# Kernel optimization log

Hardware: AMD Instinct MI355X
Metric: run time of the kernel (lower is better)

The kernel has to match this reference:

```python
import jax, jax.numpy as jnp
import numpy as np
from jax import lax

S = 8  # num_segments


def conv2d(x, w, stride=1, pad=0):
    return lax.conv_general_dilated(x, w, (stride, stride), [(pad, pad), (pad, pad)],
                                    dimension_numbers=('NCHW', 'OIHW', 'NCHW'))


def bn(x, g, b):  # inference-mode BatchNorm as per-channel affine
    return x * g[None, :, None, None] + b[None, :, None, None]


def conv1x1(x, w):  # w: [O, C]
    return jnp.einsum('bchw,oc->bohw', x, w)


def avgpool3s2(x):  # AvgPool2d(3, stride=2, padding=1), count_include_pad=True
    s = lax.reduce_window(x, 0.0, lax.add, (1, 1, 3, 3), (1, 1, 2, 2),
                          [(0, 0), (0, 0), (1, 1), (1, 1)])
    return s / 9.0


def navigation_mask(x, gumbel, nav_w, nav_bn_g, nav_bn_b, gs_w, gs_b, temp=1.0):
    B = x.shape[0]
    y = x.mean(axis=(2, 3))                                    # global avg pool -> [B, C]
    g = jnp.maximum(y @ nav_w.T * nav_bn_g + nav_bn_b, 0.0)    # conv_pool (1x1) + BN + ReLU -> [B, 2]
    g = g.reshape(B // S, S, 2)
    # grouped 1x1 conv (groups=S) == per-segment 2x2 matmul; gs_w: [S, out, in]
    logits = jnp.einsum('bsi,sji->bsj', g, gs_w) + gs_b        # [nvid, S, 2]
    y_soft = jax.nn.softmax((logits + gumbel) / temp, axis=-1)
    hard = jax.nn.one_hot(jnp.argmax(y_soft, axis=-1), 2, dtype=y_soft.dtype)
    y_st = hard + y_soft - lax.stop_gradient(y_soft)           # straight-through hard gumbel
    return y_st[:, :, 1].reshape(B, 1, 1, 1)                   # channel 1 = focal-on


def setup_inputs() -> dict:
    key = jax.random.key(0)
    ks = iter(jax.random.split(key, 48))

    def rn(shape, scale=0.05):
        return jax.random.normal(next(ks), shape, dtype=jnp.float32) * scale

    B, C_in, C_out, C_amp, H = 128, 64, 128, 64, 56
    u = jax.random.uniform(next(ks), (B // S, S, 2), minval=1e-6, maxval=1.0 - 1e-6)
    return dict(
        x=rn((B, C_in, H, H), 1.0),
        gumbel=(-jnp.log(-jnp.log(u))).astype(jnp.float32),
        nav_w=rn((2, C_in)), nav_bn_g=jnp.ones((2,), jnp.float32), nav_bn_b=jnp.zeros((2,), jnp.float32),
        gs_w=rn((S, 2, 2)),
        gs_b=jnp.tile(jnp.array([1.0, 10.0], dtype=jnp.float32), (S, 1)),  # bias init from source
        ba_w1=rn((C_amp, C_in, 3, 3)), ba_g1=jnp.ones((C_amp,), jnp.float32), ba_b1=jnp.zeros((C_amp,), jnp.float32),
        ba_w2=rn((C_amp, C_amp, 3, 3)), ba_g2=jnp.ones((C_amp,), jnp.float32), ba_b2=jnp.zeros((C_amp,), jnp.float32),
        bf_wd=rn((C_out, C_in)), bf_gd=jnp.ones((C_out,), jnp.float32), bf_bd=jnp.zeros((C_out,), jnp.float32),
        bf_w1=rn((C_out, C_in, 3, 3)), bf_g1=jnp.ones((C_out,), jnp.float32), bf_b1=jnp.zeros((C_out,), jnp.float32),
        bf_w2=rn((C_out, C_out, 3, 3)), bf_g2=jnp.ones((C_out,), jnp.float32), bf_b2=jnp.zeros((C_out,), jnp.float32),
        bt_w=rn((C_out, C_amp)), bt_g=jnp.ones((C_out,), jnp.float32), bt_b=jnp.zeros((C_out,), jnp.float32),
        att_w1=rn((C_out // 16, C_out), 0.01), att_w2=rn((C_out, C_out // 16), 0.01),
        fu_w1=rn((C_out, C_out, 3, 3)), fu_g1=jnp.ones((C_out,), jnp.float32), fu_b1=jnp.zeros((C_out,), jnp.float32),
        fu_w2=rn((C_out, C_out, 3, 3)), fu_g2=jnp.ones((C_out,), jnp.float32), fu_b2=jnp.zeros((C_out,), jnp.float32),
    )


def reference(x, gumbel, nav_w, nav_bn_g, nav_bn_b, gs_w, gs_b,
              ba_w1, ba_g1, ba_b1, ba_w2, ba_g2, ba_b2,
              bf_wd, bf_gd, bf_bd, bf_w1, bf_g1, bf_b1, bf_w2, bf_g2, bf_b2,
              bt_w, bt_g, bt_b, att_w1, att_w2,
              fu_w1, fu_g1, fu_b1, fu_w2, fu_g2, fu_b2):
    mask = navigation_mask(x, gumbel, nav_w, nav_bn_g, nav_bn_b, gs_w, gs_b)
    # ample branch: stride-2 low-res residual block (last_relu=False)
    res_l = avgpool3s2(x)
    h = jnp.maximum(bn(conv2d(x, ba_w1, 2, 1), ba_g1, ba_b1), 0.0)
    x_little = bn(conv2d(h, ba_w2, 1, 1), ba_g2, ba_b2) + res_l              # [B,64,28,28]
    # focal branch: full-res residual block, branch gated per-segment by mask
    res_b = bn(conv1x1(x, bf_wd), bf_gd, bf_bd)
    h = jnp.maximum(bn(conv2d(x, bf_w1, 1, 1), bf_g1, bf_b1), 0.0)
    x_big = res_b + mask * bn(conv2d(h, bf_w2, 1, 1), bf_g2, bf_b2)          # [B,128,56,56]
    x_little = bn(conv1x1(x_little, bt_w), bt_g, bt_b)
    x_little = jnp.repeat(jnp.repeat(x_little, 2, axis=2), 2, axis=3)        # F.interpolate nearest
    # SE-style dynamic fusion
    y = (x_little + x_big).mean(axis=(2, 3))                                 # [B,128]
    att = jax.nn.sigmoid(jnp.maximum(y @ att_w1.T, 0.0) @ att_w2.T)[:, :, None, None]
    out = jnp.maximum(att * x_little + (1.0 - att) * x_big, 0.0)
    # fusion block: residual, last_relu=True
    h = jnp.maximum(bn(conv2d(out, fu_w1, 1, 1), fu_g1, fu_b1), 0.0)
    out = jnp.maximum(bn(conv2d(h, fu_w2, 1, 1), fu_g2, fu_b2) + out, 0.0)
    return out, mask
```

## Files before the change

### kernel.cpp

```cpp
#include <hip/hip_runtime.h>
#include <cstdint>
#include <cstddef>

#define BLK 256

typedef __bf16 bf16x8 __attribute__((ext_vector_type(8)));
typedef float  f32x4  __attribute__((ext_vector_type(4)));

__device__ __forceinline__ float block_reduce_sum(float v, float* sm) {
#pragma unroll
  for (int off = 32; off > 0; off >>= 1) v += __shfl_down(v, off, 64);
  const int lane = threadIdx.x & 63;
  const int wid  = threadIdx.x >> 6;
  if (lane == 0) sm[wid] = v;
  __syncthreads();
  v = sm[0] + sm[1] + sm[2] + sm[3];
  __syncthreads();
  return v;
}

__global__ __launch_bounds__(BLK) void gap_x_k(const float* __restrict__ x,
                                               float* __restrict__ y) {
  __shared__ float sm[4];
  const float4* p4 = reinterpret_cast<const float4*>(x + (size_t)blockIdx.x * 3136);
  float s = 0.f;
  for (int i = threadIdx.x; i < 784; i += BLK) {
    float4 v = p4[i];
    s += (v.x + v.y) + (v.z + v.w);
  }
  s = block_reduce_sum(s, sm);
  if (threadIdx.x == 0) y[blockIdx.x] = s * (1.f / 3136.f);
}

__global__ void mask_k(const float* __restrict__ y, const float* __restrict__ gumbel,
                       const float* __restrict__ nav_w, const float* __restrict__ nbg,
                       const float* __restrict__ nbb, const float* __restrict__ gsw,
                       const float* __restrict__ gsb, float* __restrict__ maskv,
                       float* __restrict__ mask_out) {
  int b = threadIdx.x;
  float d0 = 0.f, d1 = 0.f;
  for (int c = 0; c < 64; ++c) {
    float yv = y[b * 64 + c];
    d0 += yv * nav_w[c];
    d1 += yv * nav_w[64 + c];
  }
  float g0 = fmaxf(d0 * nbg[0] + nbb[0], 0.f);
  float g1 = fmaxf(d1 * nbg[1] + nbb[1], 0.f);
  int vid = b >> 3, s = b & 7;
  float l0 = gsw[s * 4 + 0] * g0 + gsw[s * 4 + 1] * g1 + gsb[s * 2 + 0] + gumbel[(vid * 8 + s) * 2 + 0];
  float l1 = gsw[s * 4 + 2] * g0 + gsw[s * 4 + 3] * g1 + gsb[s * 2 + 1] + gumbel[(vid * 8 + s) * 2 + 1];
  float m = (l1 > l0) ? 1.f : 0.f;
  maskv[b] = m;
  mask_out[b] = m;
}

__global__ __launch_bounds__(BLK) void avgpool_k(const float* __restrict__ x,
                                                 float* __restrict__ out) {
  int idx = blockIdx.x * BLK + threadIdx.x;
  int p = idx % 784;
  int bc = idx / 784;
  int h = p / 28, w = p % 28;
  const float* xp = x + (size_t)bc * 3136;
  int h0 = 2 * h - 1, w0 = 2 * w - 1;
  float s = 0.f;
#pragma unroll
  for (int i = 0; i < 3; ++i) {
    int hh = h0 + i;
    if (hh < 0 || hh >= 56) continue;
#pragma unroll
    for (int j = 0; j < 3; ++j) {
      int ww = w0 + j;
      if (ww < 0 || ww >= 56) continue;
      s += xp[hh * 56 + ww];
    }
  }
  out[idx] = s * (1.f / 9.f);
}

template <int C>
__global__ __launch_bounds__(BLK) void txp_k(const float* __restrict__ src,
                                             __bf16* __restrict__ dst, int NP) {
  __shared__ float t[C * 65];
  const int b = blockIdx.y;
  const int p0 = blockIdx.x * 64;
  for (int i = threadIdx.x; i < C * 64; i += BLK) {
    int c = i >> 6, p = i & 63;
    float v = 0.f;
    if (p0 + p < NP) v = src[((size_t)b * C + c) * NP + p0 + p];
    t[c * 65 + p] = v;
  }
  __syncthreads();
  constexpr int CQ = C / 8;
  for (int i = threadIdx.x; i < 64 * CQ; i += BLK) {
    int cq = i % CQ, pix = i / CQ;
    if (p0 + pix < NP) {
      __bf16 o[8];
#pragma unroll
      for (int j = 0; j < 8; ++j) o[j] = (__bf16)t[(cq * 8 + j) * 65 + pix];
      *reinterpret_cast<uint4*>(dst + ((size_t)b * NP + p0 + pix) * C + cq * 8) =
          *reinterpret_cast<uint4*>(o);
    }
  }
}

__global__ void pack3_k(const float* __restrict__ w, __bf16* __restrict__ dst,
                        int CIN, int MT) {
  int total = (CIN / 32) * 9 * MT * 64;
  int idx = blockIdx.x * BLK + threadIdx.x;
  if (idx >= total) return;
  int lane = idx & 63;
  int g = idx >> 6;
  int mt = g % MT; g /= MT;
  int t = g % 9;  int q = g / 9;
  int oc = mt * 16 + (lane & 15);
  int quad = lane >> 4;
#pragma unroll
  for (int j = 0; j < 8; ++j) {
    int c = q * 32 + quad * 8 + j;
    dst[(size_t)idx * 8 + j] = (__bf16)w[((size_t)oc * CIN + c) * 9 + t];
  }
}

__global__ void pack1_k(const float* __restrict__ w, __bf16* __restrict__ dst,
                        int CIN, int MT) {
  int total = (CIN / 32) * MT * 64;
  int idx = blockIdx.x * BLK + threadIdx.x;
  if (idx >= total) return;
  int lane = idx & 63;
  int g = idx >> 6;
  int mt = g % MT;
  int q = g / MT;
  int oc = mt * 16 + (lane & 15);
  int quad = lane >> 4;
#pragma unroll
  for (int j = 0; j < 8; ++j) {
    int c = q * 32 + quad * 8 + j;
    dst[(size_t)idx * 8 + j] = (__bf16)w[(size_t)oc * CIN + c];
  }
}

template <int W_IMG, int ROWS>
struct Stage {
  static constexpr int COLS  = W_IMG + 2;
  static constexpr int NSLOT = ROWS * COLS * 4;
  static constexpr int NIT   = (NSLOT + BLK - 1) / BLK;
  uint4 R[NIT];

  __device__ __forceinline__ void load(const __bf16* __restrict__ inT, int CIN, int c0,
                                       int img, int h0) {
    constexpr int NPIX = W_IMG * W_IMG;
#pragma unroll
    for (int it = 0; it < NIT; ++it) {
      int s = threadIdx.x + it * BLK;
      uint4 v{0u, 0u, 0u, 0u};
      if (s < NSLOT) {
        int pix = s >> 2, q = s & 3;
        int r = pix / COLS, cc = pix - r * COLS;
        int gh = h0 - 1 + r, gw = cc - 1;
        if (gh >= 0 && gh < W_IMG && gw >= 0 && gw < W_IMG)
          v = *reinterpret_cast<const uint4*>(
              inT + ((size_t)img * NPIX + gh * W_IMG + gw) * CIN + c0 + q * 8);
      }
      R[it] = v;
    }
  }

  __device__ __forceinline__ void store(__bf16* lds) {
#pragma unroll
    for (int it = 0; it < NIT; ++it) {
      int s = threadIdx.x + it * BLK;
      if (s < NSLOT) {
        int pix = s >> 2, q = s & 3;
        *reinterpret_cast<uint4*>(lds + pix * 40 + q * 8) = R[it];
      }
    }
  }
};

template <int W_IMG, int CIN, int MTW, int MODE, int OUTBF>
__global__ __launch_bounds__(BLK, 2) void conv3_bf(
    const __bf16* __restrict__ inT, const __bf16* __restrict__ wp,
    const float* __restrict__ gamma, const float* __restrict__ beta,
    const float* __restrict__ res, void* __restrict__ outv) {
  constexpr int ROWS = 128 / W_IMG + 4;
  constexpr int COLS = W_IMG + 2;
  constexpr int NPIX = W_IMG * W_IMG;
  constexpr int NCH  = CIN / 32;
  constexpr int MT_TOT = MTW * 2;
  constexpr int COUT = MT_TOT * 16;
  constexpr int TILE_E = ROWS * COLS * 40;
  constexpr int LDSE = (OUTBF && 128 * COUT > TILE_E) ? 128 * COUT : TILE_E;
  __shared__ __bf16 lds[LDSE];

  const int tid = threadIdx.x;
  const int lane = tid & 63, wv = tid >> 6;
  const int wm = wv >> 1, wn = wv & 1;
  const int quad = lane >> 4, li = lane & 15;
  const int img = blockIdx.y;
  const int P0 = blockIdx.x * 128;
  const int h0 = P0 / W_IMG;

  int basee[4]; int pstore[4]; bool pok[4];
#pragma unroll
  for (int nt = 0; nt < 4; ++nt) {
    int p = P0 + wn * 64 + nt * 16 + li;
    bool ok = p < NPIX;
    int p2 = ok ? p : (NPIX - 1);
    int h = p2 / W_IMG, w = p2 - h * W_IMG;
    basee[nt] = ((h - h0) * COLS + w) * 40 + quad * 8;
    pstore[nt] = p2; pok[nt] = ok;
  }

  f32x4 acc[MTW][4];
#pragma unroll
  for (int mt = 0; mt < MTW; ++mt)
#pragma unroll
    for (int nt = 0; nt < 4; ++nt) acc[mt][nt] = (f32x4){0.f, 0.f, 0.f, 0.f};

  const bf16x8* wp8 = reinterpret_cast<const bf16x8*>(wp);

  Stage<W_IMG, ROWS> st;
  st.load(inT, CIN, 0, img, h0);
  for (int q = 0; q < NCH; ++q) {
    __syncthreads();
    st.store(lds);
    __syncthreads();
    if (q + 1 < NCH) st.load(inT, CIN, (q + 1) * 32, img, h0);
#pragma unroll
    for (int t = 0; t < 9; ++t) {
      const int toff = ((t / 3) * COLS + (t % 3)) * 40;
      bf16x8 wf[MTW];
#pragma unroll
      for (int mt = 0; mt < MTW; ++mt)
        wf[mt] = wp8[(size_t)((q * 9 + t) * MT_TOT + wm * MTW + mt) * 64 + lane];
      bf16x8 xf[4];
#pragma unroll
      for (int nt = 0; nt < 4; ++nt)
        xf[nt] = *reinterpret_cast<const bf16x8*>(&lds[basee[nt] + toff]);
#pragma unroll
      for (int mt = 0; mt < MTW; ++mt)
#pragma unroll
        for (int nt = 0; nt < 4; ++nt)
          acc[mt][nt] = __builtin_amdgcn_mfma_f32_16x16x32_bf16(wf[mt], xf[nt], acc[mt][nt], 0, 0, 0);
    }
  }

  if constexpr (!OUTBF) {
    float* out = (float*)outv;
#pragma unroll
    for (int mt = 0; mt < MTW; ++mt) {
#pragma unroll
      for (int r = 0; r < 4; ++r) {
        int oc = wm * MTW * 16 + mt * 16 + quad * 4 + r;
        float g = gamma[oc], bb = beta[oc];
#pragma unroll
        for (int nt = 0; nt < 4; ++nt) {
          if (!pok[nt]) continue;
          size_t idx = ((size_t)img * COUT + oc) * NPIX + pstore[nt];
          float v = acc[mt][nt][r] * g + bb;
          if constexpr (MODE == 1 || MODE == 2) v += res[idx];
          if constexpr (MODE == 0 || MODE == 2) v = fmaxf(v, 0.f);
          out[idx] = v;
        }
      }
    }
  } else {
    __bf16* outT = (__bf16*)outv;
    __syncthreads();
#pragma unroll
    for (int mt = 0; mt < MTW; ++mt) {
      int ocb = wm * MTW * 16 + mt * 16 + quad * 4;
      float g0 = gamma[ocb + 0], b0 = beta[ocb + 0];
      float g1 = gamma[ocb + 1], b1 = beta[ocb + 1];
      float g2 = gamma[ocb + 2], b2 = beta[ocb + 2];
      float g3 = gamma[ocb + 3], b3 = beta[ocb + 3];
#pragma unroll
      for (int nt = 0; nt < 4; ++nt) {
        if (!pok[nt]) continue;
        int pl = wn * 64 + nt * 16 + li;
        __bf16 o[4];
        o[0] = (__bf16)fmaxf(acc[mt][nt][0] * g0 + b0, 0.f);
        o[1] = (__bf16)fmaxf(acc[mt][nt][1] * g1 + b1, 0.f);
        o[2] = (__bf16)fmaxf(acc[mt][nt][2] * g2 + b2, 0.f);
        o[3] = (__bf16)fmaxf(acc[mt][nt][3] * g3 + b3, 0.f);
        int byt = pl * (COUT * 2) + ocb * 2;
        byt ^= (pl & 7) << 4;
        *reinterpret_cast<uint2*>(reinterpret_cast<char*>(lds) + byt) =
            *reinterpret_cast<uint2*>(o);
      }
    }
    __syncthreads();
    constexpr int SLOTS_ROW = COUT / 8;
    constexpr int ROWS_PASS = BLK / SLOTS_ROW;
#pragma unroll
    for (int pass = 0; pass < 128 / ROWS_PASS; ++pass) {
      int pl = pass * ROWS_PASS + (tid / SLOTS_ROW);
      int ss = tid % SLOTS_ROW;
      if (P0 + pl < NPIX) {
        int byt = pl * (COUT * 2) + ss * 16;
        byt ^= (pl & 7) << 4;
        uint4 vv = *reinterpret_cast<const uint4*>(reinterpret_cast<const char*>(lds) + byt);
        *reinterpret_cast<uint4*>(outT + ((size_t)img * NPIX + P0 + pl) * COUT + ss * 8) = vv;
      }
    }
  }
}

__global__ __launch_bounds__(BLK, 2) void conv_ba1_mfma(
    const __bf16* __restrict__ xT, const __bf16* __restrict__ wp,
    const float* __restrict__ gamma, const float* __restrict__ beta,
    __bf16* __restrict__ outT) {
  constexpr int WOUT = 28, NPIX = 784;
  constexpr int ROWS = 13, COLS = 58;
  constexpr int TILE_E = ROWS * COLS * 40;
  __shared__ __bf16 lds[TILE_E];

  const int tid = threadIdx.x;
  const int lane = tid & 63, wv = tid >> 6;
  const int wm = wv >> 1, wn = wv & 1;
  const int quad = lane >> 4, li = lane & 15;
  const int img = blockIdx.y;
  const int P0 = blockIdx.x * 128;
  const int h0 = P0 / WOUT;

  int basee[4]; bool pok[4];
#pragma unroll
  for (int nt = 0; nt < 4; ++nt) {
    int p = P0 + wn * 64 + nt * 16 + li;
    bool ok = p < NPIX;
    int p2 = ok ? p : (NPIX - 1);
    int h = p2 / WOUT, w = p2 - h * WOUT;
    basee[nt] = (2 * (h - h0) * COLS + 2 * w) * 40 + quad * 8;
    pok[nt] = ok;
  }

  f32x4 acc[2][4];
#pragma unroll
  for (int mt = 0; mt < 2; ++mt)
#pragma unroll
    for (int nt = 0; nt < 4; ++nt) acc[mt][nt] = (f32x4){0.f, 0.f, 0.f, 0.f};

  const bf16x8* wp8 = reinterpret_cast<const bf16x8*>(wp);

  Stage<56, 13> st;
  st.load(xT, 64, 0, img, 2 * h0);
  for (int q = 0; q < 2; ++q) {
    __syncthreads();
    st.store(lds);
    __syncthreads();
    if (q == 0) st.load(xT, 64, 32, img, 2 * h0);
#pragma unroll
    for (int t = 0; t < 9; ++t) {
      const int toff = ((t / 3) * COLS + (t % 3)) * 40;
      bf16x8 wf[2];
#pragma unroll
      for (int mt = 0; mt < 2; ++mt)
        wf[mt] = wp8[(size_t)((q * 9 + t) * 4 + wm * 2 + mt) * 64 + lane];
      bf16x8 xf[4];
#pragma unroll
      for (int nt = 0; nt < 4; ++nt)
        xf[nt] = *reinterpret_cast<const bf16x8*>(&lds[basee[nt] + toff]);
#pragma unroll
      for (int mt = 0; mt < 2; ++mt)
#pragma unroll
        for (int nt = 0; nt < 4; ++nt)
          acc[mt][nt] = __builtin_amdgcn_mfma_f32_16x16x32_bf16(wf[mt], xf[nt], acc[mt][nt], 0, 0, 0);
    }
  }

  __syncthreads();
#pragma unroll
  for (int mt = 0; mt < 2; ++mt) {
    int ocb = wm * 32 + mt * 16 + quad * 4;
    float g0 = gamma[ocb + 0], b0 = beta[ocb + 0];
    float g1 = gamma[ocb + 1], b1 = beta[ocb + 1];
    float g2 = gamma[ocb + 2], b2 = beta[ocb + 2];
    float g3 = gamma[ocb + 3], b3 = beta[ocb + 3];
#pragma unroll
    for (int nt = 0; nt < 4; ++nt) {
      if (!pok[nt]) continue;
      int pl = wn * 64 + nt * 16 + li;
      __bf16 o[4];
      o[0] = (__bf16)fmaxf(acc[mt][nt][0] * g0 + b0, 0.f);
      o[1] = (__bf16)fmaxf(acc[mt][nt][1] * g1 + b1, 0.f);
      o[2] = (__bf16)fmaxf(acc[mt][nt][2] * g2 + b2, 0.f);
      o[3] = (__bf16)fmaxf(acc[mt][nt][3] * g3 + b3, 0.f);
      int byt = pl * 128 + ocb * 2;
      byt ^= (pl & 7) << 4;
      *reinterpret_cast<uint2*>(reinterpret_cast<char*>(lds) + byt) =
          *reinterpret_cast<uint2*>(o);
    }
  }
  __syncthreads();
#pragma unroll
  for (int pass = 0; pass < 4; ++pass) {
    int pl = pass * 32 + (tid >> 3);
    int ss = tid & 7;
    if (P0 + pl < NPIX) {
      int byt = pl * 128 + ss * 16;
      byt ^= (pl & 7) << 4;
      uint4 vv = *reinterpret_cast<const uint4*>(reinterpret_cast<const char*>(lds) + byt);
      *reinterpret_cast<uint4*>(outT + ((size_t)img * NPIX + P0 + pl) * 64 + ss * 8) = vv;
    }
  }
}

__global__ __launch_bounds__(BLK, 2) void conv_xbig_bf(
    const __bf16* __restrict__ hfT, const __bf16* __restrict__ xT,
    const __bf16* __restrict__ wp3, const __bf16* __restrict__ wp1,
    const float* __restrict__ g2v, const float* __restrict__ b2v,
    const float* __restrict__ gdv, const float* __restrict__ bdv,
    const float* __restrict__ maskv, float* __restrict__ out) {
  constexpr int W_IMG = 56, ROWS = 6, COLS = 58, NPIX = 3136;
  __shared__ __bf16 lds[ROWS * COLS * 40];

  const int tid = threadIdx.x;
  const int lane = tid & 63, wv = tid >> 6;
  const int wm = wv >> 1, wn = wv & 1;
  const int quad = lane >> 4, li = lane & 15;
  const int img = blockIdx.y;
  const int P0 = blockIdx.x * 128;
  const int h0 = P0 / W_IMG;
  const float m = maskv[img];

  int basee[4]; int pstore[4]; bool pok[4];
#pragma unroll
  for (int nt = 0; nt < 4; ++nt) {
    int p = P0 + wn * 64 + nt * 16 + li;
    bool ok = p < NPIX;
    int p2 = ok ? p : (NPIX - 1);
    int h = p2 / W_IMG, w = p2 - h * W_IMG;
    basee[nt] = ((h - h0) * COLS + w) * 40 + quad * 8;
    pstore[nt] = p2; pok[nt] = ok;
  }

  f32x4 acc3[4][4], acc1[4][4];
#pragma unroll
  for (int mt = 0; mt < 4; ++mt)
#pragma unroll
    for (int nt = 0; nt < 4; ++nt) {
      acc3[mt][nt] = (f32x4){0.f, 0.f, 0.f, 0.f};
      acc1[mt][nt] = (f32x4){0.f, 0.f, 0.f, 0.f};
    }

  const bf16x8* wp3v = reinterpret_cast<const bf16x8*>(wp3);
  const bf16x8* wp1v = reinterpret_cast<const bf16x8*>(wp1);

  Stage<56, 6> st;
  st.load(hfT, 128, 0, img, h0);

  for (int q = 0; q < 4; ++q) {
    __syncthreads();
    st.store(lds);
    __syncthreads();
    if (q < 3) st.load(hfT, 128, (q + 1) * 32, img, h0);
    else       st.load(xT, 64, 0, img, h0);
#pragma unroll
    for (int t = 0; t < 9; ++t) {
      const int toff = ((t / 3) * COLS + (t % 3)) * 40;
      bf16x8 wf[4];
#pragma unroll
      for (int mt = 0; mt < 4; ++mt)
        wf[mt] = wp3v[(size_t)(((q * 9 + t) * 8) + wm * 4 + mt) * 64 + lane];
      bf16x8 xf[4];
#pragma unroll
      for (int nt = 0; nt < 4; ++nt)
        xf[nt] = *reinterpret_cast<const bf16x8*>(&lds[basee[nt] + toff]);
#pragma unroll
      for (int mt = 0; mt < 4; ++mt)
#pragma unroll
        for (int nt = 0; nt < 4; ++nt)
          acc3[mt][nt] = __builtin_amdgcn_mfma_f32_16x16x32_bf16(wf[mt], xf[nt], acc3[mt][nt], 0, 0, 0);
    }
  }

  for (int q = 0; q < 2; ++q) {
    __syncthreads();
    st.store(lds);
    __syncthreads();
    if (q == 0) st.load(xT, 64, 32, img, h0);
    const int toff = (1 * COLS + 1) * 40;
    bf16x8 wf[4];
#pragma unroll
    for (int mt = 0; mt < 4; ++mt)
      wf[mt] = wp1v[(size_t)((q * 8) + wm * 4 + mt) * 64 + lane];
    bf16x8 xf[4];
#pragma unroll
    for (int nt = 0; nt < 4; ++nt)
      xf[nt] = *reinterpret_cast<const bf16x8*>(&lds[basee[nt] + toff]);
#pragma unroll
    for (int mt = 0; mt < 4; ++mt)
#pragma unroll
      for (int nt = 0; nt < 4; ++nt)
        acc1[mt][nt] = __builtin_amdgcn_mfma_f32_16x16x32_bf16(wf[mt], xf[nt], acc1[mt][nt], 0, 0, 0);
  }

#pragma unroll
  for (int mt = 0; mt < 4; ++mt) {
#pragma unroll
    for (int r = 0; r < 4; ++r) {
      int oc = wm * 64 + mt * 16 + quad * 4 + r;
      float g2 = g2v[oc], b2 = b2v[oc], gd = gdv[oc], bd = bdv[oc];
#pragma unroll
      for (int nt = 0; nt < 4; ++nt) {
        if (!pok[nt]) continue;
        size_t idx = ((size_t)img * 128 + oc) * NPIX + pstore[nt];
        float v = (acc1[mt][nt][r] * gd + bd) + m * (acc3[mt][nt][r] * g2 + b2);
        out[idx] = v;
      }
    }
  }
}

__global__ __launch_bounds__(BLK) void conv1x1_bt_k(
    const float* __restrict__ xl, const float* __restrict__ w,
    const float* __restrict__ g, const float* __restrict__ bt, float* __restrict__ out) {
  const int b = blockIdx.z;
  const int oc0 = blockIdx.y * 8;
  const float* __restrict__ xp = xl + (size_t)b * 64 * 784;
  float gr[8], br[8];
#pragma unroll
  for (int j = 0; j < 8; ++j) {
    gr[j] = g[oc0 + j];
    br[j] = bt[oc0 + j];
  }
  for (int p = (int)threadIdx.x; p < 784; p += BLK) {
    float acc[8];
#pragma unroll
    for (int j = 0; j < 8; ++j) acc[j] = 0.f;
    for (int c = 0; c < 64; ++c) {
      float xv = xp[c * 784 + p];
#pragma unroll
      for (int j = 0; j < 8; ++j) acc[j] += xv * w[(oc0 + j) * 64 + c];
    }
#pragma unroll
    for (int j = 0; j < 8; ++j)
      out[(size_t)(b * 128 + oc0 + j) * 784 + p] = acc[j] * gr[j] + br[j];
  }
}

__global__ __launch_bounds__(BLK) void gap2_k(const float* __restrict__ xbig,
                                              const float* __restrict__ xlbt,
                                              float* __restrict__ ysum) {
  __shared__ float sm1[4], sm2[4];
  const int bo = blockIdx.x;
  const float4* p4 = reinterpret_cast<const float4*>(xbig + (size_t)bo * 3136);
  float s1 = 0.f;
  for (int i = threadIdx.x; i < 784; i += BLK) {
    float4 v = p4[i];
    s1 += (v.x + v.y) + (v.z + v.w);
  }
  const float4* q4 = reinterpret_cast<const float4*>(xlbt + (size_t)bo * 784);
  float s2 = 0.f;
  for (int i = threadIdx.x; i < 196; i += BLK) {
    float4 v = q4[i];
    s2 += (v.x + v.y) + (v.z + v.w);
  }
  s1 = block_reduce_sum(s1, sm1);
  s2 = block_reduce_sum(s2, sm2);
  if (threadIdx.x == 0) ysum[bo] = s1 * (1.f / 3136.f) + s2 * (1.f / 784.f);
}

__global__ void att_k(const float* __restrict__ ysum, const float* __restrict__ w1,
                      const float* __restrict__ w2, float* __restrict__ att) {
  int b = blockIdx.x;
  int t = threadIdx.x;
  __shared__ float hid[8];
  __shared__ float ybuf[128];
  ybuf[t] = ysum[b * 128 + t];
  __syncthreads();
  if (t < 8) {
    float s = 0.f;
    for (int c = 0; c < 128; ++c) s += ybuf[c] * w1[t * 128 + c];
    hid[t] = fmaxf(s, 0.f);
  }
  __syncthreads();
  float s = 0.f;
#pragma unroll
  for (int j = 0; j < 8; ++j) s += hid[j] * w2[t * 8 + j];
  att[b * 128 + t] = 1.f / (1.f + expf(-s));
}

__global__ __launch_bounds__(BLK) void se_k(const float* __restrict__ xlbt,
                                            const float* __restrict__ att,
                                            float* __restrict__ out) {
  int idx = blockIdx.x * BLK + threadIdx.x;
  int p = idx % 3136;
  int bo = idx / 3136;
  int h = p / 56, w = p % 56;
  float a = att[bo];
  float xl = xlbt[(size_t)bo * 784 + (h >> 1) * 28 + (w >> 1)];
  float xb = out[idx];
  out[idx] = fmaxf(a * xl + (1.f - a) * xb, 0.f);
}

extern "C" void kernel_launch(void* const* d_in, const int* in_sizes, int n_in,
                              void* d_out, int out_size, void* d_ws, size_t ws_size,
                              hipStream_t stream) {
  const float* x      = (const float*)d_in[0];
  const float* gumbel = (const float*)d_in[1];
  const float* nav_w  = (const float*)d_in[2];
  const float* nbg    = (const float*)d_in[3];
  const float* nbb    = (const float*)d_in[4];
  const float* gsw    = (const float*)d_in[5];
  const float* gsb    = (const float*)d_in[6];
  const float* ba_w1  = (const float*)d_in[7];
  const float* ba_g1  = (const float*)d_in[8];
  const float* ba_b1  = (const float*)d_in[9];
  const float* ba_w2  = (const float*)d_in[10];
  const float* ba_g2  = (const float*)d_in[11];
  const float* ba_b2  = (const float*)d_in[12];
  const float* bf_wd  = (const float*)d_in[13];
  const float* bf_gd  = (const float*)d_in[14];
  const float* bf_bd  = (const float*)d_in[15];
  const float* bf_w1  = (const float*)d_in[16];
  const float* bf_g1  = (const float*)d_in[17];
  const float* bf_b1  = (const float*)d_in[18];
  const float* bf_w2  = (const float*)d_in[19];
  const float* bf_g2  = (const float*)d_in[20];
  const float* bf_b2  = (const float*)d_in[21];
  const float* bt_w   = (const float*)d_in[22];
  const float* bt_g   = (const float*)d_in[23];
  const float* bt_b   = (const float*)d_in[24];
  const float* att_w1 = (const float*)d_in[25];
  const float* att_w2 = (const float*)d_in[26];
  const float* fu_w1  = (const float*)d_in[27];
  const float* fu_g1  = (const float*)d_in[28];
  const float* fu_b1  = (const float*)d_in[29];
  const float* fu_w2  = (const float*)d_in[30];
  const float* fu_g2  = (const float*)d_in[31];
  const float* fu_b2  = (const float*)d_in[32];

  float* out = (float*)d_out;
  float* ws  = (float*)d_ws;

  const size_t N_OUT = 51380224;
  float* bufA = ws;
  __bf16* hfbf  = (__bf16*)bufA;
  __bf16* hfubf = (__bf16*)bufA;
  __bf16* xbf   = (__bf16*)(bufA + 25690112);
  __bf16* outbf = (__bf16*)(bufA + 25690112);
  float* xlbt = bufA + N_OUT;
  float* resl = xlbt + 12845056;
  __bf16* habf = (__bf16*)(resl + 6422528);
  float* ygap = resl + 6422528 + 6422528;
  float* mskv = ygap + 8192;
  float* ysum = mskv + 128;
  float* attb = ysum + 16384;
  float* wend = attb + 16384;
  __bf16* wsW1 = (__bf16*)(wend);
  __bf16* wsW2 = (__bf16*)(wend + 36864);
  __bf16* wsF1 = (__bf16*)(wend + 110592);
  __bf16* wsF2 = (__bf16*)(wend + 184320);
  __bf16* wsA2 = (__bf16*)(wend + 258048);
  __bf16* wsWd = (__bf16*)(wend + 276480);
  __bf16* wsA1 = (__bf16*)(wend + 280576);
  float* mask_out = out + ((size_t)out_size - 128);

  pack3_k<<<36, BLK, 0, stream>>>(bf_w1, wsW1, 64, 8);
  pack3_k<<<72, BLK, 0, stream>>>(bf_w2, wsW2, 128, 8);
  pack3_k<<<72, BLK, 0, stream>>>(fu_w1, wsF1, 128, 8);
  pack3_k<<<72, BLK, 0, stream>>>(fu_w2, wsF2, 128, 8);
  pack3_k<<<18, BLK, 0, stream>>>(ba_w2, wsA2, 64, 4);
  pack3_k<<<18, BLK, 0, stream>>>(ba_w1, wsA1, 64, 4);
  pack1_k<<<4, BLK, 0, stream>>>(bf_wd, wsWd, 64, 8);

  txp_k<64><<<dim3(49, 128), BLK, 0, stream>>>(x, xbf, 3136);

  gap_x_k<<<8192, BLK, 0, stream>>>(x, ygap);
  mask_k<<<1, 128, 0, stream>>>(ygap, gumbel, nav_w, nbg, nbb, gsw, gsb, mskv, mask_out);

  avgpool_k<<<25088, BLK, 0, stream>>>(x, resl);
  conv_ba1_mfma<<<dim3(7, 128), BLK, 0, stream>>>(xbf, wsA1, ba_g1, ba_b1, habf);
  conv3_bf<28, 64, 2, 1, 0><<<dim3(7, 128), BLK, 0, stream>>>(
      habf, wsA2, ba_g2, ba_b2, resl, resl);
  conv1x1_bt_k<<<dim3(1, 16, 128), BLK, 0, stream>>>(resl, bt_w, bt_g, bt_b, xlbt);

  conv3_bf<56, 64, 4, 0, 1><<<dim3(25, 128), BLK, 0, stream>>>(
      xbf, wsW1, bf_g1, bf_b1, nullptr, hfbf);
  conv_xbig_bf<<<dim3(25, 128), BLK, 0, stream>>>(
      hfbf, xbf, wsW2, wsWd, bf_g2, bf_b2, bf_gd, bf_bd, mskv, out);

  gap2_k<<<16384, BLK, 0, stream>>>(out, xlbt, ysum);
  att_k<<<128, 128, 0, stream>>>(ysum, att_w1, att_w2, attb);
  se_k<<<200704, BLK, 0, stream>>>(xlbt, attb, out);

  txp_k<128><<<dim3(49, 128), BLK, 0, stream>>>(out, outbf, 3136);

  conv3_bf<56, 128, 4, 0, 1><<<dim3(25, 128), BLK, 0, stream>>>(
      outbf, wsF1, fu_g1, fu_b1, nullptr, hfubf);
  conv3_bf<56, 128, 4, 2, 0><<<dim3(25, 128), BLK, 0, stream>>>(
      hfubf, wsF2, fu_g2, fu_b2, out, out);
}
```

Measured before the change: 1.969 ms.

## Split output channels across blocks, remap block order, and preload weights into registers

The full-resolution 3x3 conv kernels now split their 128 output channels across two blocks via a third grid dimension. This doubles the block count and halves the per-wave accumulators, which should improve occupancy and wave balance. A remapping of block index to (image, tile, half) groups work with a stride of 8, presumably to spread neighbours across XCDs for L2 locality. Weights for all nine taps are prefetched into registers, double-buffered across channel chunks, with sched barriers. The cost is that each input tile is staged twice, once per channel half, and register pressure from the weight buffers goes up.

Result: faster. 1.860 ms (-5.5%).

```diff
diff --git a/kernel.cpp b/kernel.cpp
--- a/kernel.cpp
+++ b/kernel.cpp
@@ -177,8 +177,8 @@
   }
 };
 
-template <int W_IMG, int CIN, int MTW, int MODE, int OUTBF>
-__global__ __launch_bounds__(BLK, 2) void conv3_bf(
+template <int W_IMG, int CIN, int MTW, int MODE, int OUTBF, int NSPLIT>
+__global__ __launch_bounds__(BLK, 2) void conv3s_bf(
     const __bf16* __restrict__ inT, const __bf16* __restrict__ wp,
     const float* __restrict__ gamma, const float* __restrict__ beta,
     const float* __restrict__ res, void* __restrict__ outv) {
@@ -187,18 +187,30 @@
   constexpr int NPIX = W_IMG * W_IMG;
   constexpr int NCH  = CIN / 32;
   constexpr int MT_TOT = MTW * 2;
-  constexpr int COUT = MT_TOT * 16;
+  constexpr int COUT_B = MT_TOT * 16;
+  constexpr int COUT_G = COUT_B * NSPLIT;
+  constexpr int MT_TOTG = COUT_G / 16;
+  constexpr int NT = (NPIX + 127) / 128;
   constexpr int TILE_E = ROWS * COLS * 40;
-  constexpr int LDSE = (OUTBF && 128 * COUT > TILE_E) ? 128 * COUT : TILE_E;
+  constexpr int LDSE = (OUTBF && 128 * COUT_B > TILE_E) ? 128 * COUT_B : TILE_E;
   __shared__ __bf16 lds[LDSE];
 
   const int tid = threadIdx.x;
   const int lane = tid & 63, wv = tid >> 6;
   const int wm = wv >> 1, wn = wv & 1;
   const int quad = lane >> 4, li = lane & 15;
-  const int img = blockIdx.y;
-  const int P0 = blockIdx.x * 128;
+
+  const int F = blockIdx.x + NT * (blockIdx.y + 128 * blockIdx.z);
+  constexpr int TOT = NT * 128 * NSPLIT;
+  int Wk = (F & 7) * (TOT >> 3) + (F >> 3);
+  int bz, u;
+  if constexpr (NSPLIT == 2) { bz = Wk & 1; u = Wk >> 1; }
+  else                       { bz = 0;      u = Wk;      }
+  const int img  = u / NT;
+  const int tile = u - img * NT;
+  const int P0 = tile * 128;
   const int h0 = P0 / W_IMG;
+  const int mtg0 = bz * MT_TOT + wm * MTW;
 
   int basee[4]; int pstore[4]; bool pok[4];
 #pragma unroll
@@ -219,20 +231,18 @@
 
   const bf16x8* wp8 = reinterpret_cast<const bf16x8*>(wp);
 
-  Stage<W_IMG, ROWS> st;
-  st.load(inT, CIN, 0, img, h0);
-  for (int q = 0; q < NCH; ++q) {
-    __syncthreads();
-    st.store(lds);
-    __syncthreads();
-    if (q + 1 < NCH) st.load(inT, CIN, (q + 1) * 32, img, h0);
+  bf16x8 wA[9 * MTW], wB[9 * MTW];
+  auto LOADW = [&](bf16x8 (&wr)[9 * MTW], int q) {
+#pragma unroll
+    for (int t = 0; t < 9; ++t)
+#pragma unroll
+      for (int mt = 0; mt < MTW; ++mt)
+        wr[t * MTW + mt] = wp8[(size_t)((q * 9 + t) * MT_TOTG + mtg0 + mt) * 64 + lane];
+  };
+  auto TAPS = [&](const bf16x8 (&wr)[9 * MTW]) {
 #pragma unroll
     for (int t = 0; t < 9; ++t) {
       const int toff = ((t / 3) * COLS + (t % 3)) * 40;
-      bf16x8 wf[MTW];
-#pragma unroll
-      for (int mt = 0; mt < MTW; ++mt)
-        wf[mt] = wp8[(size_t)((q * 9 + t) * MT_TOT + wm * MTW + mt) * 64 + lane];
       bf16x8 xf[4];
 #pragma unroll
       for (int nt = 0; nt < 4; ++nt)
@@ -241,8 +251,25 @@
       for (int mt = 0; mt < MTW; ++mt)
 #pragma unroll
         for (int nt = 0; nt < 4; ++nt)
-          acc[mt][nt] = __builtin_amdgcn_mfma_f32_16x16x32_bf16(wf[mt], xf[nt], acc[mt][nt], 0, 0, 0);
-    }
+          acc[mt][nt] = __builtin_amdgcn_mfma_f32_16x16x32_bf16(wr[t * MTW + mt], xf[nt], acc[mt][nt], 0, 0, 0);
+    }
+  };
+
+  Stage<W_IMG, ROWS> st;
+  LOADW(wA, 0);
+  __builtin_amdgcn_sched_barrier(0);
+  st.load(inT, CIN, 0, img, h0);
+  for (int q = 0; q < NCH; q += 2) {
+    __syncthreads();
+    st.store(lds);
+    __syncthreads();
+    if (q + 1 < NCH) { st.load(inT, CIN, (q + 1) * 32, img, h0); LOADW(wB, q + 1); }
+    TAPS(wA);
+    __syncthreads();
+    st.store(lds);
+    __syncthreads();
+    if (q + 2 < NCH) { st.load(inT, CIN, (q + 2) * 32, img, h0); LOADW(wA, q + 2); }
+    TAPS(wB);
   }
 
   if constexpr (!OUTBF) {
@@ -251,12 +278,12 @@
     for (int mt = 0; mt < MTW; ++mt) {
 #pragma unroll
       for (int r = 0; r < 4; ++r) {
-        int oc = wm * MTW * 16 + mt * 16 + quad * 4 + r;
+        int oc = bz * COUT_B + wm * MTW * 16 + mt * 16 + quad * 4 + r;
         float g = gamma[oc], bb = beta[oc];
 #pragma unroll
         for (int nt = 0; nt < 4; ++nt) {
           if (!pok[nt]) continue;
-          size_t idx = ((size_t)img * COUT + oc) * NPIX + pstore[nt];
+          size_t idx = ((size_t)img * COUT_G + oc) * NPIX + pstore[nt];
           float v = acc[mt][nt][r] * g + bb;
           if constexpr (MODE == 1 || MODE == 2) v += res[idx];
           if constexpr (MODE == 0 || MODE == 2) v = fmaxf(v, 0.f);
@@ -269,11 +296,12 @@
     __syncthreads();
 #pragma unroll
     for (int mt = 0; mt < MTW; ++mt) {
-      int ocb = wm * MTW * 16 + mt * 16 + quad * 4;
-      float g0 = gamma[ocb + 0], b0 = beta[ocb + 0];
-      float g1 = gamma[ocb + 1], b1 = beta[ocb + 1];
-      float g2 = gamma[ocb + 2], b2 = beta[ocb + 2];
-      float g3 = gamma[ocb + 3], b3 = beta[ocb + 3];
+      int ocl = wm * MTW * 16 + mt * 16 + quad * 4;
+      int ocg = bz * COUT_B + ocl;
+      float g0 = gamma[ocg + 0], b0 = beta[ocg + 0];
+      float g1 = gamma[ocg + 1], b1 = beta[ocg + 1];
+      float g2 = gamma[ocg + 2], b2 = beta[ocg + 2];
+      float g3 = gamma[ocg + 3], b3 = beta[ocg + 3];
 #pragma unroll
       for (int nt = 0; nt < 4; ++nt) {
         if (!pok[nt]) continue;
@@ -283,24 +311,24 @@
         o[1] = (__bf16)fmaxf(acc[mt][nt][1] * g1 + b1, 0.f);
         o[2] = (__bf16)fmaxf(acc[mt][nt][2] * g2 + b2, 0.f);
         o[3] = (__bf16)fmaxf(acc[mt][nt][3] * g3 + b3, 0.f);
-        int byt = pl * (COUT * 2) + ocb * 2;
+        int byt = pl * (COUT_B * 2) + ocl * 2;
         byt ^= (pl & 7) << 4;
         *reinterpret_cast<uint2*>(reinterpret_cast<char*>(lds) + byt) =
             *reinterpret_cast<uint2*>(o);
       }
     }
     __syncthreads();
-    constexpr int SLOTS_ROW = COUT / 8;
+    constexpr int SLOTS_ROW = COUT_B / 8;
     constexpr int ROWS_PASS = BLK / SLOTS_ROW;
 #pragma unroll
     for (int pass = 0; pass < 128 / ROWS_PASS; ++pass) {
       int pl = pass * ROWS_PASS + (tid / SLOTS_ROW);
       int ss = tid % SLOTS_ROW;
       if (P0 + pl < NPIX) {
-        int byt = pl * (COUT * 2) + ss * 16;
+        int byt = pl * (COUT_B * 2) + ss * 16;
         byt ^= (pl & 7) << 4;
         uint4 vv = *reinterpret_cast<const uint4*>(reinterpret_cast<const char*>(lds) + byt);
-        *reinterpret_cast<uint4*>(outT + ((size_t)img * NPIX + P0 + pl) * COUT + ss * 8) = vv;
+        *reinterpret_cast<uint4*>(outT + ((size_t)img * NPIX + P0 + pl) * COUT_G + bz * COUT_B + ss * 8) = vv;
       }
     }
   }
@@ -342,20 +370,23 @@
 
   const bf16x8* wp8 = reinterpret_cast<const bf16x8*>(wp);
 
+  bf16x8 wr[18];
   Stage<56, 13> st;
   st.load(xT, 64, 0, img, 2 * h0);
   for (int q = 0; q < 2; ++q) {
     __syncthreads();
     st.store(lds);
     __syncthreads();
+#pragma unroll
+    for (int t = 0; t < 9; ++t)
+#pragma unroll
+      for (int mt = 0; mt < 2; ++mt)
+        wr[t * 2 + mt] = wp8[(size_t)((q * 9 + t) * 4 + wm * 2 + mt) * 64 + lane];
+    __builtin_amdgcn_sched_barrier(0);
     if (q == 0) st.load(xT, 64, 32, img, 2 * h0);
 #pragma unroll
     for (int t = 0; t < 9; ++t) {
       const int toff = ((t / 3) * COLS + (t % 3)) * 40;
-      bf16x8 wf[2];
-#pragma unroll
-      for (int mt = 0; mt < 2; ++mt)
-        wf[mt] = wp8[(size_t)((q * 9 + t) * 4 + wm * 2 + mt) * 64 + lane];
       bf16x8 xf[4];
 #pragma unroll
       for (int nt = 0; nt < 4; ++nt)
@@ -364,7 +395,7 @@
       for (int mt = 0; mt < 2; ++mt)
 #pragma unroll
         for (int nt = 0; nt < 4; ++nt)
-          acc[mt][nt] = __builtin_amdgcn_mfma_f32_16x16x32_bf16(wf[mt], xf[nt], acc[mt][nt], 0, 0, 0);
+          acc[mt][nt] = __builtin_amdgcn_mfma_f32_16x16x32_bf16(wr[t * 2 + mt], xf[nt], acc[mt][nt], 0, 0, 0);
     }
   }
 
@@ -411,15 +442,22 @@
     const float* __restrict__ g2v, const float* __restrict__ b2v,
     const float* __restrict__ gdv, const float* __restrict__ bdv,
     const float* __restrict__ maskv, float* __restrict__ out) {
-  constexpr int W_IMG = 56, ROWS = 6, COLS = 58, NPIX = 3136;
+  constexpr int W_IMG = 56, ROWS = 6, COLS = 58, NPIX = 3136, NT = 25;
   __shared__ __bf16 lds[ROWS * COLS * 40];
 
   const int tid = threadIdx.x;
   const int lane = tid & 63, wv = tid >> 6;
   const int wm = wv >> 1, wn = wv & 1;
   const int quad = lane >> 4, li = lane & 15;
-  const int img = blockIdx.y;
-  const int P0 = blockIdx.x * 128;
+
+  const int F = blockIdx.x + NT * (blockIdx.y + 128 * blockIdx.z);
+  constexpr int TOT = NT * 128 * 2;
+  int Wk = (F & 7) * (TOT >> 3) + (F >> 3);
+  const int bz = Wk & 1;
+  const int u  = Wk >> 1;
+  const int img  = u / NT;
+  const int tile = u - img * NT;
+  const int P0 = tile * 128;
   const int h0 = P0 / W_IMG;
   const float m = maskv[img];
 
@@ -434,9 +472,9 @@
     pstore[nt] = p2; pok[nt] = ok;
   }
 
-  f32x4 acc3[4][4], acc1[4][4];
-#pragma unroll
-  for (int mt = 0; mt < 4; ++mt)
+  f32x4 acc3[2][4], acc1[2][4];
+#pragma unroll
+  for (int mt = 0; mt < 2; ++mt)
 #pragma unroll
     for (int nt = 0; nt < 4; ++nt) {
       acc3[mt][nt] = (f32x4){0.f, 0.f, 0.f, 0.f};
@@ -446,6 +484,7 @@
   const bf16x8* wp3v = reinterpret_cast<const bf16x8*>(wp3);
   const bf16x8* wp1v = reinterpret_cast<const bf16x8*>(wp1);
 
+  bf16x8 wr[18];
   Stage<56, 6> st;
   st.load(hfT, 128, 0, img, h0);
 
@@ -453,24 +492,26 @@
     __syncthreads();
     st.store(lds);
     __syncthreads();
+#pragma unroll
+    for (int t = 0; t < 9; ++t)
+#pragma unroll
+      for (int mt = 0; mt < 2; ++mt)
+        wr[t * 2 + mt] = wp3v[(size_t)((q * 9 + t) * 8 + bz * 4 + wm * 2 + mt) * 64 + lane];
+    __builtin_amdgcn_sched_barrier(0);
     if (q < 3) st.load(hfT, 128, (q + 1) * 32, img, h0);
     else       st.load(xT, 64, 0, img, h0);
 #pragma unroll
     for (int t = 0; t < 9; ++t) {
       const int toff = ((t / 3) * COLS + (t % 3)) * 40;
-      bf16x8 wf[4];
-#pragma unroll
-      for (int mt = 0; mt < 4; ++mt)
-        wf[mt] = wp3v[(size_t)(((q * 9 + t) * 8) + wm * 4 + mt) * 64 + lane];
       bf16x8 xf[4];
 #pragma unroll
       for (int nt = 0; nt < 4; ++nt)
         xf[nt] = *reinterpret_cast<const bf16x8*>(&lds[basee[nt] + toff]);
 #pragma unroll
-      for (int mt = 0; mt < 4; ++mt)
+      for (int mt = 0; mt < 2; ++mt)
 #pragma unroll
         for (int nt = 0; nt < 4; ++nt)
-          acc3[mt][nt] = __builtin_amdgcn_mfma_f32_16x16x32_bf16(wf[mt], xf[nt], acc3[mt][nt], 0, 0, 0);
+          acc3[mt][nt] = __builtin_amdgcn_mfma_f32_16x16x32_bf16(wr[t * 2 + mt], xf[nt], acc3[mt][nt], 0, 0, 0);
     }
   }
 
@@ -478,28 +519,29 @@
     __syncthreads();
     st.store(lds);
     __syncthreads();
+    bf16x8 w1[2];
+#pragma unroll
+    for (int mt = 0; mt < 2; ++mt)
+      w1[mt] = wp1v[(size_t)(q * 8 + bz * 4 + wm * 2 + mt) * 64 + lane];
+    __builtin_amdgcn_sched_barrier(0);
     if (q == 0) st.load(xT, 64, 32, img, h0);
     const int toff = (1 * COLS + 1) * 40;
-    bf16x8 wf[4];
-#pragma unroll
-    for (int mt = 0; mt < 4; ++mt)
-      wf[mt] = wp1v[(size_t)((q * 8) + wm * 4 + mt) * 64 + lane];
     bf16x8 xf[4];
 #pragma unroll
     for (int nt = 0; nt < 4; ++nt)
       xf[nt] = *reinterpret_cast<const bf16x8*>(&lds[basee[nt] + toff]);
 #pragma unroll
-    for (int mt = 0; mt < 4; ++mt)
+    for (int mt = 0; mt < 2; ++mt)
 #pragma unroll
       for (int nt = 0; nt < 4; ++nt)
-        acc1[mt][nt] = __builtin_amdgcn_mfma_f32_16x16x32_bf16(wf[mt], xf[nt], acc1[mt][nt], 0, 0, 0);
-  }
-
-#pragma unroll
-  for (int mt = 0; mt < 4; ++mt) {
+        acc1[mt][nt] = __builtin_amdgcn_mfma_f32_16x16x32_bf16(w1[mt], xf[nt], acc1[mt][nt], 0, 0, 0);
+  }
+
+#pragma unroll
+  for (int mt = 0; mt < 2; ++mt) {
 #pragma unroll
     for (int r = 0; r < 4; ++r) {
-      int oc = wm * 64 + mt * 16 + quad * 4 + r;
+      int oc = bz * 64 + wm * 32 + mt * 16 + quad * 4 + r;
       float g2 = g2v[oc], b2 = b2v[oc], gd = gdv[oc], bd = bdv[oc];
 #pragma unroll
       for (int nt = 0; nt < 4; ++nt) {
@@ -672,13 +714,13 @@
 
   avgpool_k<<<25088, BLK, 0, stream>>>(x, resl);
   conv_ba1_mfma<<<dim3(7, 128), BLK, 0, stream>>>(xbf, wsA1, ba_g1, ba_b1, habf);
-  conv3_bf<28, 64, 2, 1, 0><<<dim3(7, 128), BLK, 0, stream>>>(
+  conv3s_bf<28, 64, 2, 1, 0, 1><<<dim3(7, 128), BLK, 0, stream>>>(
       habf, wsA2, ba_g2, ba_b2, resl, resl);
   conv1x1_bt_k<<<dim3(1, 16, 128), BLK, 0, stream>>>(resl, bt_w, bt_g, bt_b, xlbt);
 
-  conv3_bf<56, 64, 4, 0, 1><<<dim3(25, 128), BLK, 0, stream>>>(
+  conv3s_bf<56, 64, 2, 0, 1, 2><<<dim3(25, 128, 2), BLK, 0, stream>>>(
       xbf, wsW1, bf_g1, bf_b1, nullptr, hfbf);
-  conv_xbig_bf<<<dim3(25, 128), BLK, 0, stream>>>(
+  conv_xbig_bf<<<dim3(25, 128, 2), BLK, 0, stream>>>(
       hfbf, xbf, wsW2, wsWd, bf_g2, bf_b2, bf_gd, bf_bd, mskv, out);
 
   gap2_k<<<16384, BLK, 0, stream>>>(out, xlbt, ysum);
@@ -687,8 +729,8 @@
 
   txp_k<128><<<dim3(49, 128), BLK, 0, stream>>>(out, outbf, 3136);
 
-  conv3_bf<56, 128, 4, 0, 1><<<dim3(25, 128), BLK, 0, stream>>>(
+  conv3s_bf<56, 128, 2, 0, 1, 2><<<dim3(25, 128, 2), BLK, 0, stream>>>(
       outbf, wsF1, fu_g1, fu_b1, nullptr, hfubf);
-  conv3_bf<56, 128, 4, 2, 0><<<dim3(25, 128), BLK, 0, stream>>>(
+  conv3s_bf<56, 128, 2, 2, 0, 2><<<dim3(25, 128, 2), BLK, 0, stream>>>(
       hfubf, wsF2, fu_g2, fu_b2, out, out);
 }
```
